# Optimization experiments

Measured on AMD Instinct MI355X. Metric: run time of the kernel, lower is better.

Reference implementation:

```python
import jax, jax.numpy as jnp
import numpy as np

B, CIN, COUT, H, W = 16, 64, 64, 256, 256
MX, MY = 64, 64  # retained spectral modes (NxW, NyW)
NY_R = W // 2 + 1  # rfft length of last dim


def _dequant(q, scale, min_val):
    # matches torch: (q.float() + 127) * scale + min_val, q in [-127, 128]
    return (q.astype(jnp.float32) + 127.0) * scale + min_val


def setup_inputs() -> dict:
    key = jax.random.key(0)
    k0, k1, k2, k3 = jax.random.split(key, 4)
    x = jax.random.normal(k0, (B, CIN, H, W), dtype=jnp.float32)
    q_real = jax.random.randint(k1, (CIN, COUT, MX, MY), -127, 129, dtype=jnp.int32)
    q_imag = jax.random.randint(k2, (CIN, COUT, MX, MY), -127, 129, dtype=jnp.int32)
    q_bias = jax.random.randint(k3, (COUT,), -127, 129, dtype=jnp.int32)
    return {
        "x": x,
        "q_real": q_real,
        "q_imag": q_imag,
        "q_bias": q_bias,
        "scale_real": jnp.float32(2e-3),
        "min_real": jnp.float32(-0.25),
        "scale_imag": jnp.float32(2e-3),
        "min_imag": jnp.float32(-0.25),
        "b_scale": jnp.float32(1e-4),
        "b_min": jnp.float32(-0.0128),
    }


def reference(x, q_real, q_imag, q_bias, scale_real, min_real, scale_imag, min_imag, b_scale, b_min):
    # 1) rFFT over the last two (spatial) dims, norm='backward' (torch default)
    x_fft = jnp.fft.rfftn(x, axes=(-2, -1), norm="backward")  # [B, Cin, H, NY_R] complex

    # 2) inline dequantize the complex spectral weight
    w_real = _dequant(q_real, scale_real, min_real)
    w_imag = _dequant(q_imag, scale_imag, min_imag)
    Wc = jax.lax.complex(w_real, w_imag)  # [Cin, Cout, MX, MY]

    # 3) center slices as in the torch forward
    cx, nx = H // 2, MX // 2
    sx = slice(cx - nx, cx + (MX - nx))
    cy, ny = NY_R // 2, MY // 2
    sy = slice(cy - ny, cy + (MY - ny))

    # fused channel multiply-accumulate (replaces the nested python loop)
    out_slice = jnp.einsum("bixy,ioxy->boxy", x_fft[:, :, sx, sy], Wc)

    out_fft = jnp.zeros((B, COUT, H, NY_R), dtype=x_fft.dtype)
    out_fft = out_fft.at[:, :, sx, sy].set(out_slice)

    # 4) inverse rFFT back to spatial domain
    x_out = jnp.fft.irfftn(out_fft, s=(H, W), axes=(-2, -1), norm="backward")

    # 5) dequantized bias, broadcast over (1, Cout, 1, 1)
    bias = _dequant(q_bias, b_scale, b_min)
    return x_out + bias[None, :, None, None]
```

## Files before the change

### kernel.cpp

```cpp
#include <hip/hip_runtime.h>


#define HW    256
#define NCIN  64
#define NCOUT 64
#define NB    16
#define R0    96
#define C0    32

typedef __bf16 bf16x8 __attribute__((ext_vector_type(8)));
typedef float  f32x4  __attribute__((ext_vector_type(4)));

__device__ __forceinline__ unsigned short f2bf(float f) {
    unsigned u = __float_as_uint(f);
    unsigned r = (u + 0x7FFFu + ((u >> 16) & 1u)) >> 16;
    return (unsigned short)r;
}
__device__ __forceinline__ bf16x8 ld_frag_g(const unsigned short* p) {
    return __builtin_bit_cast(bf16x8, *(const uint4*)p);
}
__device__ __forceinline__ unsigned pk2(float a, float b) {
    return (unsigned)f2bf(a) | ((unsigned)f2bf(b) << 16);
}
__device__ __forceinline__ void gload_lds16(const unsigned short* g, unsigned short* l) {
    __builtin_amdgcn_global_load_lds(
        (const __attribute__((address_space(1))) unsigned int*)g,
        (__attribute__((address_space(3))) unsigned int*)l, 16, 0, 0);
}

__global__ void build_tables2(unsigned short* __restrict__ A1tab,
                              unsigned short* __restrict__ B2T) {
    int idx = blockIdx.x * 256 + threadIdx.x;
    int h = idx >> 7;
    int k = idx & 127;
    int kk = k & 63;
    const float TPO = 0.0245436926061702596754f;
    float s, c;
    int m1 = (((R0 + kk) * h) & 255);
    sincosf((float)m1 * TPO, &s, &c);
    A1tab[idx] = f2bf(k < 64 ? c : s);
    int m2 = (((C0 + kk) * h) & 255);
    sincosf((float)m2 * TPO, &s, &c);
    B2T[idx] = f2bf(k < 64 ? c : -s);
}

__global__ void build_fwd_tables(unsigned short* __restrict__ B1fT,
                                 unsigned short* __restrict__ A2f) {
    int idx = blockIdx.x * 256 + threadIdx.x;
    const float TPO = 0.0245436926061702596754f;
    float s, c;
    if (idx < 32768) {
        int cc = idx >> 8, w = idx & 255;
        int m = (((C0 + (cc & 63)) * w) & 255);
        sincosf((float)m * TPO, &s, &c);
        int sidx = (cc << 8) | (w ^ ((cc & 7) << 3));
        B1fT[sidx] = f2bf(cc < 64 ? c : -s);
    } else {
        int j = idx - 32768;
        int mr = j >> 9, k = j & 511;
        int m = (((R0 + (mr & 63)) * (k & 255)) & 255);
        sincosf((float)m * TPO, &s, &c);
        float v = (mr < 64) ? ((k < 256) ? c : s)
                            : ((k < 256) ? -s : c);
        A2f[j] = f2bf(v);
    }
}

__global__ __launch_bounds__(256, 2) void fwd_mfma(
        const float*          __restrict__ x,
        const unsigned short* __restrict__ B1fT,
        const unsigned short* __restrict__ A2f,
        float*                __restrict__ Xout) {
    __shared__ __align__(16) unsigned short smem[32768];
    int bi = blockIdx.x;
    const float* xim = x + (size_t)bi * 65536;
    int t = threadIdx.x, lane = t & 63, wv = t >> 6;
    int g = lane >> 4, lr = lane & 15;

    #pragma unroll
    for (int i = 0; i < 16; ++i)
        gload_lds16(B1fT + i * 2048 + t * 8, &smem[i * 2048 + wv * 512]);

    const float* xrow[4];
    #pragma unroll
    for (int mf = 0; mf < 4; ++mf)
        xrow[mf] = xim + (wv * 64 + mf * 16 + lr) * 256 + g * 8;
    float4 xv[2][4][2];
    #pragma unroll
    for (int mf = 0; mf < 4; ++mf) {
        xv[0][mf][0] = *(const float4*)(xrow[mf]);
        xv[0][mf][1] = *(const float4*)(xrow[mf] + 4);
    }
    __syncthreads();

    f32x4 acc[4][8];
    #pragma unroll
    for (int mf = 0; mf < 4; ++mf)
        #pragma unroll
        for (int nf = 0; nf < 8; ++nf) acc[mf][nf] = (f32x4)0.0f;

    #pragma unroll
    for (int ks = 0; ks < 8; ++ks) {
        const int cur = ks & 1;
        if (ks < 7) {
            #pragma unroll
            for (int mf = 0; mf < 4; ++mf) {
                xv[cur ^ 1][mf][0] = *(const float4*)(xrow[mf] + (ks + 1) * 32);
                xv[cur ^ 1][mf][1] = *(const float4*)(xrow[mf] + (ks + 1) * 32 + 4);
            }
        }
        int k0 = ks * 32 + g * 8;
        bf16x8 b[8];
        #pragma unroll
        for (int nf = 0; nf < 8; ++nf) {
            int n = nf * 16 + lr;
            b[nf] = __builtin_bit_cast(bf16x8,
                      *(const uint4*)&smem[n * 256 + (k0 ^ ((n & 7) << 3))]);
        }
        bf16x8 a[4];
        #pragma unroll
        for (int mf = 0; mf < 4; ++mf) {
            uint4 pk;
            pk.x = pk2(xv[cur][mf][0].x, xv[cur][mf][0].y);
            pk.y = pk2(xv[cur][mf][0].z, xv[cur][mf][0].w);
            pk.z = pk2(xv[cur][mf][1].x, xv[cur][mf][1].y);
            pk.w = pk2(xv[cur][mf][1].z, xv[cur][mf][1].w);
            a[mf] = __builtin_bit_cast(bf16x8, pk);
        }
        #pragma unroll
        for (int mf = 0; mf < 4; ++mf)
            #pragma unroll
            for (int nf = 0; nf < 8; ++nf)
                acc[mf][nf] = __builtin_amdgcn_mfma_f32_16x16x32_bf16(
                                  a[mf], b[nf], acc[mf][nf], 0, 0, 0);
    }
    __syncthreads();

    #pragma unroll
    for (int mf = 0; mf < 4; ++mf)
        #pragma unroll
        for (int nf = 0; nf < 8; ++nf) {
            int cl  = nf * 16 + lr;
            int col = cl & 63;
            int h0  = wv * 64 + mf * 16 + g * 4;
            int kk0 = (cl < 64) ? h0 : (256 + h0);
            uint2 pk;
            pk.x = pk2(acc[mf][nf][0], acc[mf][nf][1]);
            pk.y = pk2(acc[mf][nf][2], acc[mf][nf][3]);
            *(uint2*)&smem[col * 512 + (kk0 ^ ((col & 7) << 3))] = pk;
        }
    __syncthreads();

    f32x4 acc2[2][4];
    #pragma unroll
    for (int mf = 0; mf < 2; ++mf)
        #pragma unroll
        for (int nf = 0; nf < 4; ++nf) acc2[mf][nf] = (f32x4)0.0f;
    #pragma unroll
    for (int ks = 0; ks < 16; ++ks) {
        int k0 = ks * 32 + g * 8;
        bf16x8 a2[2], b2[4];
        #pragma unroll
        for (int mf = 0; mf < 2; ++mf) {
            int m = wv * 32 + mf * 16 + lr;
            a2[mf] = ld_frag_g(A2f + m * 512 + k0);
        }
        #pragma unroll
        for (int nf = 0; nf < 4; ++nf) {
            int c = nf * 16 + lr;
            b2[nf] = __builtin_bit_cast(bf16x8,
                       *(const uint4*)&smem[c * 512 + (k0 ^ ((c & 7) << 3))]);
        }
        #pragma unroll
        for (int mf = 0; mf < 2; ++mf)
            #pragma unroll
            for (int nf = 0; nf < 4; ++nf)
                acc2[mf][nf] = __builtin_amdgcn_mfma_f32_16x16x32_bf16(
                                   a2[mf], b2[nf], acc2[mf][nf], 0, 0, 0);
    }
    float* Xp = Xout + (size_t)bi * 8192;
    #pragma unroll
    for (int mf = 0; mf < 2; ++mf)
        #pragma unroll
        for (int nf = 0; nf < 4; ++nf)
            #pragma unroll
            for (int rg = 0; rg < 4; ++rg) {
                int m = wv * 32 + mf * 16 + g * 4 + rg;
                int c = nf * 16 + lr;
                Xp[(m >> 6) * 4096 + (m & 63) * 64 + c] = acc2[mf][nf][rg];
            }
}

__global__ __launch_bounds__(256) void mix_kernel(
        const float* __restrict__ X,
        const int*   __restrict__ q_real,
        const int*   __restrict__ q_imag,
        const float* __restrict__ s_r, const float* __restrict__ m_r,
        const float* __restrict__ s_i, const float* __restrict__ m_i,
        float2*      __restrict__ Y) {
    int rr = blockIdx.x;
    int ot = blockIdx.y;
    int t  = threadIdx.x;
    int c  = t & 63;
    int oq = t >> 6;
    int o  = ot * 4 + oq;
    float sr = *s_r, mr = *m_r, si = *s_i, mi = *m_i;
    __shared__ __align__(16) float2 xsh[16][64];
    float Yr[16], Yi[16];
    #pragma unroll
    for (int b = 0; b < 16; ++b) { Yr[b] = 0.f; Yi[b] = 0.f; }
    for (int i = 0; i < NCIN; ++i) {
        __syncthreads();
        #pragma unroll
        for (int l = t; l < 1024; l += 256) {
            int b = l >> 6, cc = l & 63;
            size_t base = (size_t)(b * NCIN + i) * 8192 + rr * 64 + cc;
            xsh[b][cc] = make_float2(X[base], X[base + 4096]);
        }
        __syncthreads();
        int widx = ((i * NCOUT + o) * 64 + rr) * 64 + c;
        float wr = (float)(q_real[widx] + 127) * sr + mr;
        float wi = (float)(q_imag[widx] + 127) * si + mi;
        #pragma unroll
        for (int b = 0; b < 16; ++b) {
            float2 xv = xsh[b][c];
            Yr[b] += xv.x * wr - xv.y * wi;
            Yi[b] += xv.x * wi + xv.y * wr;
        }
    }
    #pragma unroll
    for (int b = 0; b < 16; ++b)
        Y[(((size_t)b * NCOUT + o) * 64 + rr) * 64 + c] = make_float2(Yr[b], Yi[b]);
}

__global__ __launch_bounds__(256, 2) void inv_mfma(
        const float2*         __restrict__ Y,
        const unsigned short* __restrict__ A1tab,
        const unsigned short* __restrict__ B2T,
        const int*            __restrict__ q_bias,
        const float* __restrict__ b_s, const float* __restrict__ b_m,
        float*                __restrict__ out) {
    __shared__ __align__(16) unsigned short smem[32768];
    int bo   = blockIdx.x;
    int t    = threadIdx.x;
    int lane = t & 63;
    int wv   = t >> 6;
    int g    = lane >> 4;
    int lr   = lane & 15;
    float bias = ((float)q_bias[bo & 63] + 127.0f) * (*b_s) + (*b_m);

    const float2* Yp = Y + (size_t)bo * 4096;
    for (int l = t; l < 4096; l += 256) {
        int r = l >> 6, c = l & 63;
        float2 y = Yp[l];
        unsigned short yr  = f2bf(y.x);
        unsigned short yi  = f2bf(y.y);
        unsigned short nyi = f2bf(-y.y);
        int sw = (c & 7) << 3;
        smem[c * 128        + ((r)      ^ sw)] = yr;
        smem[c * 128        + ((64 + r) ^ sw)] = nyi;
        smem[(64 + c) * 128 + ((r)      ^ sw)] = yi;
        smem[(64 + c) * 128 + ((64 + r) ^ sw)] = yr;
    }
    __syncthreads();

    f32x4 acc[4][8];
    #pragma unroll
    for (int mf = 0; mf < 4; ++mf)
        #pragma unroll
        for (int nf = 0; nf < 8; ++nf) acc[mf][nf] = (f32x4)0.0f;

    #pragma unroll
    for (int ks = 0; ks < 4; ++ks) {
        int k0 = ks * 32 + g * 8;
        bf16x8 a[4], b[8];
        #pragma unroll
        for (int mf = 0; mf < 4; ++mf) {
            int h = wv * 64 + mf * 16 + lr;
            a[mf] = ld_frag_g(A1tab + h * 128 + k0);
        }
        #pragma unroll
        for (int nf = 0; nf < 8; ++nf) {
            int n = nf * 16 + lr;
            b[nf] = ld_frag_g(&smem[n * 128 + (k0 ^ ((n & 7) << 3))]);
        }
        #pragma unroll
        for (int mf = 0; mf < 4; ++mf)
            #pragma unroll
            for (int nf = 0; nf < 8; ++nf)
                acc[mf][nf] = __builtin_amdgcn_mfma_f32_16x16x32_bf16(
                                  a[mf], b[nf], acc[mf][nf], 0, 0, 0);
    }
    __syncthreads();

    #pragma unroll
    for (int mf = 0; mf < 4; ++mf)
        #pragma unroll
        for (int nf = 0; nf < 8; ++nf)
            #pragma unroll
            for (int rg = 0; rg < 4; ++rg) {
                int h = wv * 64 + mf * 16 + g * 4 + rg;
                int k = nf * 16 + lr;
                smem[h * 128 + (k ^ ((h & 7) << 3))] = f2bf(acc[mf][nf][rg]);
            }
    __syncthreads();

    const float scale = 2.0f / 65536.0f;
    float* outp = out + (size_t)bo * 65536;
    #pragma unroll
    for (int nh = 0; nh < 2; ++nh) {
        f32x4 acc2[4][8];
        #pragma unroll
        for (int mf = 0; mf < 4; ++mf)
            #pragma unroll
            for (int nf = 0; nf < 8; ++nf) acc2[mf][nf] = (f32x4)0.0f;

        #pragma unroll
        for (int ks = 0; ks < 4; ++ks) {
            int k0 = ks * 32 + g * 8;
            bf16x8 a[4], b[8];
            #pragma unroll
            for (int mf = 0; mf < 4; ++mf) {
                int h = wv * 64 + mf * 16 + lr;
                a[mf] = ld_frag_g(&smem[h * 128 + (k0 ^ ((h & 7) << 3))]);
            }
            #pragma unroll
            for (int nf = 0; nf < 8; ++nf) {
                int w = nh * 128 + nf * 16 + lr;
                b[nf] = ld_frag_g(B2T + w * 128 + k0);
            }
            #pragma unroll
            for (int mf = 0; mf < 4; ++mf)
                #pragma unroll
                for (int nf = 0; nf < 8; ++nf)
                    acc2[mf][nf] = __builtin_amdgcn_mfma_f32_16x16x32_bf16(
                                       a[mf], b[nf], acc2[mf][nf], 0, 0, 0);
        }
        #pragma unroll
        for (int mf = 0; mf < 4; ++mf)
            #pragma unroll
            for (int rg = 0; rg < 4; ++rg) {
                int h = wv * 64 + mf * 16 + g * 4 + rg;
                float* row = outp + h * 256 + nh * 128 + lr;
                #pragma unroll
                for (int nf = 0; nf < 8; ++nf)
                    row[nf * 16] = acc2[mf][nf][rg] * scale + bias;
            }
    }
}

extern "C" void kernel_launch(void* const* d_in, const int* in_sizes, int n_in,
                              void* d_out, int out_size, void* d_ws, size_t ws_size,
                              hipStream_t stream) {
    const float* x          = (const float*)d_in[0];
    const int*   q_real     = (const int*)  d_in[1];
    const int*   q_imag     = (const int*)  d_in[2];
    const int*   q_bias     = (const int*)  d_in[3];
    const float* scale_real = (const float*)d_in[4];
    const float* min_real   = (const float*)d_in[5];
    const float* scale_imag = (const float*)d_in[6];
    const float* min_imag   = (const float*)d_in[7];
    const float* b_scale    = (const float*)d_in[8];
    const float* b_min      = (const float*)d_in[9];
    float* out = (float*)d_out;

    float* ws = (float*)d_ws;
    unsigned short* A1tab = (unsigned short*)(ws);
    unsigned short* B2T   = (unsigned short*)(ws + 16384);
    unsigned short* B1fT  = (unsigned short*)(ws + 32768);
    unsigned short* A2f   = (unsigned short*)(ws + 49152);
    float*          Xws   = (float*) (ws + 81920);
    float2*         Yws   = (float2*)(ws + 81920 + 8388608);

    build_tables2<<<128, 256, 0, stream>>>(A1tab, B2T);
    build_fwd_tables<<<384, 256, 0, stream>>>(B1fT, A2f);
    fwd_mfma<<<NB * NCIN, 256, 0, stream>>>(x, B1fT, A2f, Xws);
    mix_kernel<<<dim3(64, 16), 256, 0, stream>>>(Xws, q_real, q_imag,
                                                 scale_real, min_real,
                                                 scale_imag, min_imag, Yws);
    inv_mfma<<<NB * NCOUT, 256, 0, stream>>>(Yws, A1tab, B2T,
                                             q_bias, b_scale, b_min, out);
}
```

Baseline: 332.0 us.

## Double-buffer and register-block the spectral channel-mix kernel

Rewrites the channel-mixing kernel so each thread computes two adjacent modes for 8 output channels per block instead of one mode for 4, halving the grid. The X tile now uses separate real/imag shared buffers, double-buffered and filled with float4 loads prefetched one input channel ahead, and the int2 weight loads are prefetched two channels ahead, so there is one barrier per iteration instead of two. The aim is to cut load latency stalls and per-element load count, and to halve re-reads of X across output-channel groups. In exchange each thread holds more accumulator registers and there are half as many blocks.

```diff
diff --git a/kernel.cpp b/kernel.cpp
--- a/kernel.cpp
+++ b/kernel.cpp
@@ -201,36 +201,76 @@
     int rr = blockIdx.x;
     int ot = blockIdx.y;
     int t  = threadIdx.x;
-    int c  = t & 63;
-    int oq = t >> 6;
-    int o  = ot * 4 + oq;
+    int cp = t & 31;
+    int oq = t >> 5;
+    int o  = ot * 8 + oq;
+    int c0 = cp * 2;
     float sr = *s_r, mr = *m_r, si = *s_i, mi = *m_i;
-    __shared__ __align__(16) float2 xsh[16][64];
-    float Yr[16], Yi[16];
-    #pragma unroll
-    for (int b = 0; b < 16; ++b) { Yr[b] = 0.f; Yi[b] = 0.f; }
-    for (int i = 0; i < NCIN; ++i) {
-        __syncthreads();
-        #pragma unroll
-        for (int l = t; l < 1024; l += 256) {
-            int b = l >> 6, cc = l & 63;
-            size_t base = (size_t)(b * NCIN + i) * 8192 + rr * 64 + cc;
-            xsh[b][cc] = make_float2(X[base], X[base + 4096]);
-        }
-        __syncthreads();
-        int widx = ((i * NCOUT + o) * 64 + rr) * 64 + c;
-        float wr = (float)(q_real[widx] + 127) * sr + mr;
-        float wi = (float)(q_imag[widx] + 127) * si + mi;
+
+    __shared__ float xr_sh[2][16][72];
+    __shared__ float xi_sh[2][16][72];
+
+    int sb  = t >> 4;
+    int scq = t & 15;
+    const float* xbase = X + (size_t)sb * 64 * 8192 + rr * 64 + scq * 4;
+
+    const int* qrp = q_real + (size_t)o * 4096 + rr * 64 + c0;
+    const int* qip = q_imag + (size_t)o * 4096 + rr * 64 + c0;
+
+    float Yr0[16], Yi0[16], Yr1[16], Yi1[16];
+    #pragma unroll
+    for (int b = 0; b < 16; ++b) { Yr0[b] = 0.f; Yi0[b] = 0.f; Yr1[b] = 0.f; Yi1[b] = 0.f; }
+
+    int2 wqr[2], wqi[2];
+    wqr[0] = *(const int2*)(qrp);
+    wqi[0] = *(const int2*)(qip);
+    wqr[1] = *(const int2*)(qrp + 262144);
+    wqi[1] = *(const int2*)(qip + 262144);
+    {
+        float4 gr = *(const float4*)(xbase);
+        float4 gi = *(const float4*)(xbase + 4096);
+        *(float4*)&xr_sh[0][sb][scq * 4] = gr;
+        *(float4*)&xi_sh[0][sb][scq * 4] = gi;
+    }
+    __syncthreads();
+
+    #pragma unroll 2
+    for (int i = 0; i < 64; ++i) {
+        const int cur = i & 1;
+        float4 gr, gi;
+        if (i < 63) {
+            gr = *(const float4*)(xbase + (size_t)(i + 1) * 8192);
+            gi = *(const float4*)(xbase + (size_t)(i + 1) * 8192 + 4096);
+        }
+        float wr0 = (float)(wqr[cur].x + 127) * sr + mr;
+        float wr1 = (float)(wqr[cur].y + 127) * sr + mr;
+        float wi0 = (float)(wqi[cur].x + 127) * si + mi;
+        float wi1 = (float)(wqi[cur].y + 127) * si + mi;
+        if (i < 62) {
+            wqr[cur] = *(const int2*)(qrp + (size_t)(i + 2) * 262144);
+            wqi[cur] = *(const int2*)(qip + (size_t)(i + 2) * 262144);
+        }
         #pragma unroll
         for (int b = 0; b < 16; ++b) {
-            float2 xv = xsh[b][c];
-            Yr[b] += xv.x * wr - xv.y * wi;
-            Yi[b] += xv.x * wi + xv.y * wr;
-        }
-    }
-    #pragma unroll
-    for (int b = 0; b < 16; ++b)
-        Y[(((size_t)b * NCOUT + o) * 64 + rr) * 64 + c] = make_float2(Yr[b], Yi[b]);
+            float2 xr = *(const float2*)&xr_sh[cur][b][c0];
+            float2 xi = *(const float2*)&xi_sh[cur][b][c0];
+            Yr0[b] += xr.x * wr0 - xi.x * wi0;
+            Yi0[b] += xr.x * wi0 + xi.x * wr0;
+            Yr1[b] += xr.y * wr1 - xi.y * wi1;
+            Yi1[b] += xr.y * wi1 + xi.y * wr1;
+        }
+        if (i < 63) {
+            *(float4*)&xr_sh[cur ^ 1][sb][scq * 4] = gr;
+            *(float4*)&xi_sh[cur ^ 1][sb][scq * 4] = gi;
+            __syncthreads();
+        }
+    }
+
+    #pragma unroll
+    for (int b = 0; b < 16; ++b) {
+        float4 v = make_float4(Yr0[b], Yi0[b], Yr1[b], Yi1[b]);
+        *(float4*)&Y[(size_t)b * 262144 + (size_t)o * 4096 + rr * 64 + c0] = v;
+    }
 }
 
 __global__ __launch_bounds__(256, 2) void inv_mfma(
@@ -375,9 +415,9 @@
     build_tables2<<<128, 256, 0, stream>>>(A1tab, B2T);
     build_fwd_tables<<<384, 256, 0, stream>>>(B1fT, A2f);
     fwd_mfma<<<NB * NCIN, 256, 0, stream>>>(x, B1fT, A2f, Xws);
-    mix_kernel<<<dim3(64, 16), 256, 0, stream>>>(Xws, q_real, q_imag,
-                                                 scale_real, min_real,
-                                                 scale_imag, min_imag, Yws);
+    mix_kernel<<<dim3(64, 8), 256, 0, stream>>>(Xws, q_real, q_imag,
+                                                scale_real, min_real,
+                                                scale_imag, min_imag, Yws);
     inv_mfma<<<NB * NCOUT, 256, 0, stream>>>(Yws, A1tab, B2T,
                                              q_bias, b_scale, b_min, out);
 }
```

New measurement: 270.8 us. 18.4% less time.
